# Kernel tuning notes

Measured on AMD Instinct MI355X. Metric: run time of the kernel, lower is better.

## Reference

```python
import jax, jax.numpy as jnp
import numpy as np
from jax import lax

B, T, I, H = 128, 512, 300, 256


def setup_inputs() -> dict:
    key = jax.random.key(0)
    ks = jax.random.split(key, 10)
    k = 1.0 / np.sqrt(H)
    u = lambda kk, shape: jax.random.uniform(kk, shape, jnp.float32, -k, k)
    return {
        "x": jax.random.normal(ks[0], (B, T, I), jnp.float32),
        "W_ih_f": u(ks[1], (4 * H, I)),
        "W_hh_f": u(ks[2], (4 * H, H)),
        "b_f": u(ks[3], (4 * H,)),
        "W_ih_b": u(ks[4], (4 * H, I)),
        "W_hh_b": u(ks[5], (4 * H, H)),
        "b_b": u(ks[6], (4 * H,)),
        "W_lin": u(ks[7], (2, 2 * H)),
        "b_lin": u(ks[8], (2,)),
    }


def _lstm_dir(x, W_ih, W_hh, b, reverse):
    # Precompute input projections for all timesteps: [B, T, 4H]
    xp = jnp.einsum("bti,gi->btg", x, W_ih) + b
    if reverse:
        xp = xp[:, ::-1]
    h0 = jnp.zeros((x.shape[0], H), x.dtype)
    c0 = jnp.zeros((x.shape[0], H), x.dtype)

    def step(carry, xt):
        h, c = carry
        g = xt + h @ W_hh.T  # [B, 4H]
        i_g, f_g, g_g, o_g = jnp.split(g, 4, axis=-1)  # torch gate order i,f,g,o
        i_g = jax.nn.sigmoid(i_g)
        f_g = jax.nn.sigmoid(f_g)
        g_g = jnp.tanh(g_g)
        o_g = jax.nn.sigmoid(o_g)
        c = f_g * c + i_g * g_g
        h = o_g * jnp.tanh(c)
        return (h, c), h

    _, hs = lax.scan(step, (h0, c0), jnp.swapaxes(xp, 0, 1))  # [T, B, H]
    hs = jnp.swapaxes(hs, 0, 1)  # [B, T, H]
    if reverse:
        hs = hs[:, ::-1]
    return hs


def reference(x, W_ih_f, W_hh_f, b_f, W_ih_b, W_hh_b, b_b, W_lin, b_lin):
    hf = _lstm_dir(x, W_ih_f, W_hh_f, b_f, reverse=False)  # [B, T, H]
    hb = _lstm_dir(x, W_ih_b, W_hh_b, b_b, reverse=True)   # [B, T, H]
    last = jnp.concatenate([hf[:, -1], hb[:, -1]], axis=-1)  # [B, 2H]
    return last @ W_lin.T + b_lin  # [B, 2]
```

## Files before the change

kernel.cpp:

```cpp
#include <hip/hip_runtime.h>
#include <cstdint>
#include <cstddef>

typedef _Float16 half2v __attribute__((ext_vector_type(2)));
typedef _Float16 half4v __attribute__((ext_vector_type(4)));
typedef _Float16 half8v __attribute__((ext_vector_type(8)));
typedef float f32x4 __attribute__((ext_vector_type(4)));

#if __has_builtin(__builtin_amdgcn_fdot2)
#define FDOT2(a, b, c) __builtin_amdgcn_fdot2((a), (b), (c), false)
#else
static __device__ __forceinline__ float fdot2_fb(half2v a, half2v b, float c) {
    return c + (float)a[0] * (float)b[0] + (float)a[1] * (float)b[1];
}
#define FDOT2(a, b, c) fdot2_fb((a), (b), (c))
#endif

#define SV2(v, i0, i1) __builtin_shufflevector((v), (v), (i0), (i1))

__device__ __forceinline__ float sigm(float x) { return 1.0f / (1.0f + __expf(-x)); }
__device__ __forceinline__ float tanh_(float x) { return 1.0f - 2.0f / (__expf(2.0f * x) + 1.0f); }

#define BB 128
#define TT 512
#define II 300
#define IIP 320
#define HH 256
#define GG 1024

__global__ __launch_bounds__(256) void cvt_xw(
    const float* __restrict__ X, const float* __restrict__ W,
    _Float16* __restrict__ Xh, _Float16* __restrict__ Wh)
{
    const int total = (65536 + 1024) * 40;
    for (int c = blockIdx.x * 256 + threadIdx.x; c < total; c += gridDim.x * 256) {
        const int row = c / 40;
        const int ch = c - row * 40;
        const int k0 = ch * 8;
        const float* src;
        _Float16* dst;
        if (row < 65536) {
            src = X + (size_t)row * II;
            dst = Xh + (size_t)row * IIP;
        } else {
            src = W + (size_t)(row - 65536) * II;
            dst = Wh + (size_t)(row - 65536) * IIP;
        }
        half8v hv;
        if (k0 + 8 <= II) {
            float4 a = *(const float4*)(src + k0);
            float4 b = *(const float4*)(src + k0 + 4);
            hv = half8v{(_Float16)a.x, (_Float16)a.y, (_Float16)a.z, (_Float16)a.w,
                        (_Float16)b.x, (_Float16)b.y, (_Float16)b.z, (_Float16)b.w};
        } else {
#pragma unroll
            for (int q = 0; q < 8; ++q) {
                const int k = k0 + q;
                hv[q] = (k < II) ? (_Float16)src[k] : (_Float16)0.f;
            }
        }
        *(half8v*)(dst + k0) = hv;
    }
}

#if __has_builtin(__builtin_amdgcn_global_load_lds)
#define HAVE_GLL 1
__device__ __forceinline__ void gll16(const _Float16* g, _Float16* l) {
    __builtin_amdgcn_global_load_lds(
        (const __attribute__((address_space(1))) void*)g,
        (__attribute__((address_space(3))) void*)l, 16, 0, 0);
}
#else
#define HAVE_GLL 0
#endif

__global__ __launch_bounds__(256) void gemm_xp_h(
    const _Float16* __restrict__ Xh, const _Float16* __restrict__ Wh,
    const float* __restrict__ bias, _Float16* __restrict__ XP)
{
    __shared__ __align__(16) _Float16 As[128 * 32];
    __shared__ __align__(16) _Float16 Bs[128 * 32];

    const int t = threadIdx.x;
    const int m0 = blockIdx.y * 128;
    const int n0 = blockIdx.x * 128;
    const int lane = t & 63;
    const int wv = t >> 6;
    const int mq = (wv >> 1) * 4;
    const int nq = (wv & 1) * 4;

    int rowd[2], k4d[2], cidx[2];
#pragma unroll
    for (int r = 0; r < 2; ++r) {
        const int c = wv * 128 + r * 64 + lane;
        cidx[r] = c;
        rowd[r] = ((c >> 6) << 4) | (c & 15);
        k4d[r] = (c >> 4) & 3;
    }

    f32x4 acc[4][4];
#pragma unroll
    for (int i = 0; i < 4; ++i)
#pragma unroll
        for (int j = 0; j < 4; ++j) acc[i][j] = f32x4{0.f, 0.f, 0.f, 0.f};

    for (int kc = 0; kc < IIP; kc += 32) {
        __syncthreads();
#pragma unroll
        for (int r = 0; r < 2; ++r) {
            const _Float16* ga = Xh + (size_t)(m0 + rowd[r]) * IIP + kc + k4d[r] * 8;
            const _Float16* gb = Wh + (size_t)(n0 + rowd[r]) * IIP + kc + k4d[r] * 8;
#if HAVE_GLL
            gll16(ga, &As[cidx[r] * 8]);
            gll16(gb, &Bs[cidx[r] * 8]);
#else
            *(half8v*)(&As[cidx[r] * 8]) = *(const half8v*)ga;
            *(half8v*)(&Bs[cidx[r] * 8]) = *(const half8v*)gb;
#endif
        }
        __syncthreads();

        half8v af[4], bf[4];
#pragma unroll
        for (int i = 0; i < 4; ++i) {
            af[i] = *(const half8v*)(&As[(mq + i) * 512 + (lane >> 4) * 128 + (lane & 15) * 8]);
            bf[i] = *(const half8v*)(&Bs[(nq + i) * 512 + (lane >> 4) * 128 + (lane & 15) * 8]);
        }
#pragma unroll
        for (int i = 0; i < 4; ++i)
#pragma unroll
            for (int j = 0; j < 4; ++j)
                acc[i][j] = __builtin_amdgcn_mfma_f32_16x16x32_f16(af[i], bf[j], acc[i][j], 0, 0, 0);
    }

#pragma unroll
    for (int j = 0; j < 4; ++j) {
        const int n = n0 + (nq + j) * 16 + (lane & 15);
        const float bv = bias[n];
#pragma unroll
        for (int i = 0; i < 4; ++i) {
#pragma unroll
            for (int r = 0; r < 4; ++r) {
                const int m = m0 + (mq + i) * 16 + (lane >> 4) * 4 + r;
                XP[(size_t)m * GG + n] = (_Float16)(acc[i][j][r] + bv);
            }
        }
    }
}

__global__ __launch_bounds__(256, 3) void gemm_xp(
    const float* __restrict__ X, const float* __restrict__ W,
    const float* __restrict__ bias, _Float16* __restrict__ XP)
{
    __shared__ _Float16 As[128 * 32];
    __shared__ _Float16 Bs[128 * 32];

    const int t = threadIdx.x;
    const int m0 = blockIdx.y * 128;
    const int n0 = blockIdx.x * 128;
    const int kpos = t & 7;
    const int rbase = t >> 3;
    const int lane = t & 63;
    const int wv = t >> 6;
    const int mq = (wv >> 1) * 4;
    const int nq = (wv & 1) * 4;

    f32x4 acc[4][4];
#pragma unroll
    for (int i = 0; i < 4; ++i)
#pragma unroll
        for (int j = 0; j < 4; ++j) acc[i][j] = f32x4{0.f, 0.f, 0.f, 0.f};

    for (int kc = 0; kc < 320; kc += 32) {
        __syncthreads();
        const int k0 = kc + kpos * 4;
#pragma unroll
        for (int rr = 0; rr < 4; ++rr) {
            const int row = rbase + rr * 32;
            float4 va = {0.f, 0.f, 0.f, 0.f}, vb = {0.f, 0.f, 0.f, 0.f};
            if (k0 < 300) {
                va = *(const float4*)(X + (size_t)(m0 + row) * II + k0);
                vb = *(const float4*)(W + (size_t)(n0 + row) * II + k0);
            }
            const int idx = (row >> 4) * 512 + (kpos >> 1) * 128 + (row & 15) * 8 + (kpos & 1) * 4;
            half4v ha = {(_Float16)va.x, (_Float16)va.y, (_Float16)va.z, (_Float16)va.w};
            half4v hb = {(_Float16)vb.x, (_Float16)vb.y, (_Float16)vb.z, (_Float16)vb.w};
            *(half4v*)(&As[idx]) = ha;
            *(half4v*)(&Bs[idx]) = hb;
        }
        __syncthreads();

        half8v af[4], bf[4];
#pragma unroll
        for (int i = 0; i < 4; ++i) {
            af[i] = *(const half8v*)(&As[(mq + i) * 512 + (lane >> 4) * 128 + (lane & 15) * 8]);
            bf[i] = *(const half8v*)(&Bs[(nq + i) * 512 + (lane >> 4) * 128 + (lane & 15) * 8]);
        }
#pragma unroll
        for (int i = 0; i < 4; ++i)
#pragma unroll
            for (int j = 0; j < 4; ++j)
                acc[i][j] = __builtin_amdgcn_mfma_f32_16x16x32_f16(af[i], bf[j], acc[i][j], 0, 0, 0);
    }

#pragma unroll
    for (int j = 0; j < 4; ++j) {
        const int n = n0 + (nq + j) * 16 + (lane & 15);
        const float bv = bias[n];
#pragma unroll
        for (int i = 0; i < 4; ++i) {
#pragma unroll
            for (int r = 0; r < 4; ++r) {
                const int m = m0 + (mq + i) * 16 + (lane >> 4) * 4 + r;
                XP[(size_t)m * GG + n] = (_Float16)(acc[i][j][r] + bv);
            }
        }
    }
}

__global__ __attribute__((amdgpu_flat_work_group_size(1024, 1024), amdgpu_waves_per_eu(4, 4)))
void lstm_fwd(
    const float* __restrict__ Whh, const _Float16* __restrict__ XP,
    float* __restrict__ HF)
{
    __shared__ _Float16 wlds[8 * 1024 * 8];
    __shared__ __align__(16) _Float16 hlds[2][HH];

    const int t = threadIdx.x;
    const int b = blockIdx.x;
    const int l = t & 63;
    const int wv = t >> 6;
    const int gate = l >> 4;
    const int j = wv * 16 + (l & 15);
    const int row = gate * 256 + j;
    const bool gb0 = (gate & 1) != 0;
    const bool gb1 = (gate & 2) != 0;

    half2v w[96];
    {
        const float* wr = Whh + (size_t)row * HH;
#pragma unroll
        for (int i = 0; i < 48; ++i) {
            float4 v = *(const float4*)(wr + i * 4);
            w[2 * i]     = half2v{(_Float16)v.x, (_Float16)v.y};
            w[2 * i + 1] = half2v{(_Float16)v.z, (_Float16)v.w};
        }
    }
#pragma unroll
    for (int grp = 0; grp < 8; ++grp) {
        float4 a  = *(const float4*)(Whh + (size_t)t * HH + 192 + grp * 8);
        float4 c4 = *(const float4*)(Whh + (size_t)t * HH + 192 + grp * 8 + 4);
        half8v hv = {(_Float16)a.x, (_Float16)a.y, (_Float16)a.z, (_Float16)a.w,
                     (_Float16)c4.x, (_Float16)c4.y, (_Float16)c4.z, (_Float16)c4.w};
        *(half8v*)(&wlds[grp * 8192 + t * 8]) = hv;
    }
    if (t < HH) hlds[0][t] = (_Float16)0.f;
    float c = 0.0f;
    __syncthreads();

    const _Float16* xq = XP + (size_t)b * TT * GG + row;
    _Float16 x = *xq;

    for (int ts = 0; ts < TT; ++ts) {
        const int p = ts & 1;
        const _Float16* hrd = &hlds[p][0];
        const _Float16* xn = xq + ((ts < TT - 1) ? GG : 0);
        const _Float16 nx = *xn;

        float aLo = 0.f, aHi = 0.f;
#pragma unroll
        for (int cq = 0; cq < 12; ++cq) {
            half8v hv = *(const half8v*)(&hrd[cq * 8]);
            aLo = FDOT2(SV2(hv, 0, 1), w[cq * 4 + 0], aLo);
            aLo = FDOT2(SV2(hv, 2, 3), w[cq * 4 + 1], aLo);
            aLo = FDOT2(SV2(hv, 4, 5), w[cq * 4 + 2], aLo);
            aLo = FDOT2(SV2(hv, 6, 7), w[cq * 4 + 3], aLo);
        }
#pragma unroll
        for (int cq = 12; cq < 24; ++cq) {
            half8v hv = *(const half8v*)(&hrd[cq * 8]);
            aHi = FDOT2(SV2(hv, 0, 1), w[cq * 4 + 0], aHi);
            aHi = FDOT2(SV2(hv, 2, 3), w[cq * 4 + 1], aHi);
            aHi = FDOT2(SV2(hv, 4, 5), w[cq * 4 + 2], aHi);
            aHi = FDOT2(SV2(hv, 6, 7), w[cq * 4 + 3], aHi);
        }
#pragma unroll
        for (int grp = 0; grp < 8; ++grp) {
            half8v hv = *(const half8v*)(&hrd[192 + grp * 8]);
            half8v wl = *(const half8v*)(&wlds[grp * 8192 + row * 8]);
            if (grp & 1) {
                aHi = FDOT2(SV2(hv, 0, 1), SV2(wl, 0, 1), aHi);
                aHi = FDOT2(SV2(hv, 2, 3), SV2(wl, 2, 3), aHi);
                aHi = FDOT2(SV2(hv, 4, 5), SV2(wl, 4, 5), aHi);
                aHi = FDOT2(SV2(hv, 6, 7), SV2(wl, 6, 7), aHi);
            } else {
                aLo = FDOT2(SV2(hv, 0, 1), SV2(wl, 0, 1), aLo);
                aLo = FDOT2(SV2(hv, 2, 3), SV2(wl, 2, 3), aLo);
                aLo = FDOT2(SV2(hv, 4, 5), SV2(wl, 4, 5), aLo);
                aLo = FDOT2(SV2(hv, 6, 7), SV2(wl, 6, 7), aLo);
            }
        }

        const float pre = aLo + aHi + (float)x;
        const float e1 = __shfl_xor(pre, 16, 64);
        const float e2 = __shfl_xor(pre, 32, 64);
        const float e3 = __shfl_xor(pre, 48, 64);
        const float t01 = gb0 ? e1 : pre;
        const float t10 = gb0 ? pre : e1;
        const float t23 = gb0 ? e3 : e2;
        const float t32 = gb0 ? e2 : e3;
        const float gi = gb1 ? t23 : t01;
        const float gf = gb1 ? t32 : t10;
        const float gg = gb1 ? t01 : t23;
        const float go = gb1 ? t10 : t32;

        c = sigm(gf) * c + sigm(gi) * tanh_(gg);
        const float h = sigm(go) * tanh_(c);

        if (gate == 0) {
            hlds[p ^ 1][j] = (_Float16)h;
            if (ts == TT - 1) HF[(size_t)b * HH + j] = h;
        }
        __syncthreads();

        x = nx;
        xq = xn;
    }
}

__global__ __launch_bounds__(256) void lstm_bwd(
    const float* __restrict__ X, const float* __restrict__ Wih,
    const float* __restrict__ bb, float* __restrict__ HB)
{
    __shared__ float xs[II];
    const int b = blockIdx.x, t = threadIdx.x;
    const float* xrow = X + ((size_t)b * TT + (TT - 1)) * II;
    if (t < 75) *(float4*)(&xs[t * 4]) = *(const float4*)(xrow + t * 4);
    __syncthreads();
    if (t < HH) {
        float ai = 0.f, ag = 0.f, ao = 0.f;
        const float4* wi = (const float4*)(Wih + (size_t)t * II);
        const float4* wg = (const float4*)(Wih + (size_t)(t + 512) * II);
        const float4* wo = (const float4*)(Wih + (size_t)(t + 768) * II);
        for (int k4 = 0; k4 < 75; ++k4) {
            float4 xv = *(const float4*)(&xs[k4 * 4]);
            float4 a = wi[k4], g4 = wg[k4], o4 = wo[k4];
            ai += xv.x * a.x + xv.y * a.y + xv.z * a.z + xv.w * a.w;
            ag += xv.x * g4.x + xv.y * g4.y + xv.z * g4.z + xv.w * g4.w;
            ao += xv.x * o4.x + xv.y * o4.y + xv.z * o4.z + xv.w * o4.w;
        }
        ai += bb[t];
        ag += bb[t + 512];
        ao += bb[t + 768];
        const float cg = sigm(ai) * tanh_(ag);
        HB[(size_t)b * HH + t] = sigm(ao) * tanh_(cg);
    }
}

__global__ __launch_bounds__(256) void final_k(
    const float* __restrict__ HF, const float* __restrict__ HB,
    const float* __restrict__ Wlin, const float* __restrict__ blin,
    float* __restrict__ OUT)
{
    const int t = threadIdx.x;
    const int b = t >> 1, jj = t & 1;
    float acc = blin[jj];
    const float* wf = Wlin + jj * 512;
    const float* wb = Wlin + jj * 512 + 256;
    const float* hf = HF + (size_t)b * HH;
    const float* hb = HB + (size_t)b * HH;
    for (int k = 0; k < HH; k += 4) {
        float4 h4 = *(const float4*)(hf + k);
        float4 w4 = *(const float4*)(wf + k);
        float4 g4 = *(const float4*)(hb + k);
        float4 v4 = *(const float4*)(wb + k);
        acc += h4.x * w4.x + h4.y * w4.y + h4.z * w4.z + h4.w * w4.w;
        acc += g4.x * v4.x + g4.y * v4.y + g4.z * v4.z + g4.w * v4.w;
    }
    OUT[b * 2 + jj] = acc;
}

extern "C" void kernel_launch(void* const* d_in, const int* in_sizes, int n_in,
                              void* d_out, int out_size, void* d_ws, size_t ws_size,
                              hipStream_t stream)
{
    const float* x = (const float*)d_in[0];
    const float* Wihf = (const float*)d_in[1];
    const float* Whhf = (const float*)d_in[2];
    const float* bf = (const float*)d_in[3];
    const float* Wihb = (const float*)d_in[4];
    const float* Whhb = (const float*)d_in[5];
    const float* bbv = (const float*)d_in[6];
    const float* Wlin = (const float*)d_in[7];
    const float* blin = (const float*)d_in[8];
    float* out = (float*)d_out;
    (void)Whhb; (void)in_sizes; (void)n_in; (void)out_size;

    const size_t XP_B = (size_t)BB * TT * GG * 2;
    const size_t H_B  = (size_t)BB * HH * 4;
    const size_t XH_B = (size_t)65536 * IIP * 2;
    const size_t WH_B = (size_t)GG * IIP * 2;

    _Float16* xp = (_Float16*)d_ws;
    float* hf = (float*)((char*)d_ws + XP_B);
    float* hb = hf + (size_t)BB * HH;
    _Float16* Xh = (_Float16*)((char*)d_ws + XP_B + 2 * H_B);
    _Float16* Wh = Xh + (size_t)65536 * IIP;

    lstm_bwd<<<BB, 256, 0, stream>>>(x, Wihb, bbv, hb);
    if (ws_size >= XP_B + 2 * H_B + XH_B + WH_B) {
        cvt_xw<<<2048, 256, 0, stream>>>(x, Wihf, Xh, Wh);
        gemm_xp_h<<<dim3(GG / 128, (BB * TT) / 128), 256, 0, stream>>>(Xh, Wh, bf, xp);
    } else {
        gemm_xp<<<dim3(GG / 128, (BB * TT) / 128), 256, 0, stream>>>(x, Wihf, bf, xp);
    }
    lstm_fwd<<<BB, 1024, 0, stream>>>(Whhf, xp, hf);
    final_k<<<1, 256, 0, stream>>>(hf, hb, Wlin, blin, out);
}
```

Before: 1.538 ms.

## Batch 16 sequences per block and compute recurrent matvec with MFMA

The forward LSTM recurrence changes from one batch row per 1024-thread block, using fdot2 dot products, to 16 batch rows per 512-thread block, using 16x16x32 f16 MFMA instructions. Three quarters of W_hh sit in registers as MFMA B fragments and the rest sit in LDS. Hidden state is kept in a swizzled LDS layout, and the gate nonlinearities are applied directly on the accumulator layout. This amortises weight reads over 16 sequences and uses matrix cores, but launches only 8 blocks, so per-step latency on a few CUs now sets the runtime.

```diff
diff --git a/kernel.cpp b/kernel.cpp
--- a/kernel.cpp
+++ b/kernel.cpp
@@ -6,17 +6,6 @@
 typedef _Float16 half4v __attribute__((ext_vector_type(4)));
 typedef _Float16 half8v __attribute__((ext_vector_type(8)));
 typedef float f32x4 __attribute__((ext_vector_type(4)));
-
-#if __has_builtin(__builtin_amdgcn_fdot2)
-#define FDOT2(a, b, c) __builtin_amdgcn_fdot2((a), (b), (c), false)
-#else
-static __device__ __forceinline__ float fdot2_fb(half2v a, half2v b, float c) {
-    return c + (float)a[0] * (float)b[0] + (float)a[1] * (float)b[1];
-}
-#define FDOT2(a, b, c) fdot2_fb((a), (b), (c))
-#endif
-
-#define SV2(v, i0, i1) __builtin_shufflevector((v), (v), (i0), (i1))
 
 __device__ __forceinline__ float sigm(float x) { return 1.0f / (1.0f + __expf(-x)); }
 __device__ __forceinline__ float tanh_(float x) { return 1.0f - 2.0f / (__expf(2.0f * x) + 1.0f); }
@@ -218,113 +207,113 @@
     }
 }
 
-__global__ __attribute__((amdgpu_flat_work_group_size(1024, 1024), amdgpu_waves_per_eu(4, 4)))
+__global__ __attribute__((amdgpu_flat_work_group_size(512, 512), amdgpu_waves_per_eu(2, 2)))
 void lstm_fwd(
     const float* __restrict__ Whh, const _Float16* __restrict__ XP,
     float* __restrict__ HF)
 {
-    __shared__ _Float16 wlds[8 * 1024 * 8];
-    __shared__ __align__(16) _Float16 hlds[2][HH];
+    __shared__ __align__(16) _Float16 wlds[65536];
+    __shared__ __align__(16) _Float16 hl[2][4096];
 
     const int t = threadIdx.x;
-    const int b = blockIdx.x;
+    const int b0 = blockIdx.x * 16;
     const int l = t & 63;
-    const int wv = t >> 6;
-    const int gate = l >> 4;
-    const int j = wv * 16 + (l & 15);
-    const int row = gate * 256 + j;
-    const bool gb0 = (gate & 1) != 0;
-    const bool gb1 = (gate & 2) != 0;
-
-    half2v w[96];
-    {
-        const float* wr = Whh + (size_t)row * HH;
-#pragma unroll
-        for (int i = 0; i < 48; ++i) {
-            float4 v = *(const float4*)(wr + i * 4);
-            w[2 * i]     = half2v{(_Float16)v.x, (_Float16)v.y};
-            w[2 * i + 1] = half2v{(_Float16)v.z, (_Float16)v.w};
-        }
-    }
-#pragma unroll
-    for (int grp = 0; grp < 8; ++grp) {
-        float4 a  = *(const float4*)(Whh + (size_t)t * HH + 192 + grp * 8);
-        float4 c4 = *(const float4*)(Whh + (size_t)t * HH + 192 + grp * 8 + 4);
-        half8v hv = {(_Float16)a.x, (_Float16)a.y, (_Float16)a.z, (_Float16)a.w,
-                     (_Float16)c4.x, (_Float16)c4.y, (_Float16)c4.z, (_Float16)c4.w};
-        *(half8v*)(&wlds[grp * 8192 + t * 8]) = hv;
-    }
-    if (t < HH) hlds[0][t] = (_Float16)0.f;
-    float c = 0.0f;
+    const int w = t >> 6;
+    const int n16 = l & 15;
+    const int kq = l >> 4;
+
+    half8v wr[8][6];
+#pragma unroll
+    for (int ct = 0; ct < 8; ++ct) {
+        const int nct = (ct >> 1) * 256 + w * 32 + (ct & 1) * 16;
+        const float* wp = Whh + (size_t)(nct + n16) * HH + kq * 8;
+#pragma unroll
+        for (int ks = 0; ks < 6; ++ks) {
+            float4 a = *(const float4*)(wp + ks * 32);
+            float4 b = *(const float4*)(wp + ks * 32 + 4);
+            wr[ct][ks] = half8v{(_Float16)a.x, (_Float16)a.y, (_Float16)a.z, (_Float16)a.w,
+                                (_Float16)b.x, (_Float16)b.y, (_Float16)b.z, (_Float16)b.w};
+        }
+    }
+#pragma unroll
+    for (int i = 0; i < 16; ++i) {
+        const int idx = i * 512 + t;
+        const int sn16 = idx & 15;
+        const int skq = (idx >> 4) & 3;
+        const int snt = (idx >> 6) & 63;
+        const int ss  = (idx >> 12) & 1;
+        const float* sp = Whh + (size_t)(snt * 16 + sn16) * HH + (6 + ss) * 32 + skq * 8;
+        float4 a = *(const float4*)sp;
+        float4 b = *(const float4*)(sp + 4);
+        *(half8v*)(&wlds[idx * 8]) = half8v{(_Float16)a.x, (_Float16)a.y, (_Float16)a.z, (_Float16)a.w,
+                                            (_Float16)b.x, (_Float16)b.y, (_Float16)b.z, (_Float16)b.w};
+    }
+#pragma unroll
+    for (int i = 0; i < 8; ++i) hl[0][i * 512 + t] = (_Float16)0.f;
+
+    float cst[8];
+#pragma unroll
+    for (int i = 0; i < 8; ++i) cst[i] = 0.f;
     __syncthreads();
 
-    const _Float16* xq = XP + (size_t)b * TT * GG + row;
-    _Float16 x = *xq;
-
     for (int ts = 0; ts < TT; ++ts) {
-        const int p = ts & 1;
-        const _Float16* hrd = &hlds[p][0];
-        const _Float16* xn = xq + ((ts < TT - 1) ? GG : 0);
-        const _Float16 nx = *xn;
-
-        float aLo = 0.f, aHi = 0.f;
-#pragma unroll
-        for (int cq = 0; cq < 12; ++cq) {
-            half8v hv = *(const half8v*)(&hrd[cq * 8]);
-            aLo = FDOT2(SV2(hv, 0, 1), w[cq * 4 + 0], aLo);
-            aLo = FDOT2(SV2(hv, 2, 3), w[cq * 4 + 1], aLo);
-            aLo = FDOT2(SV2(hv, 4, 5), w[cq * 4 + 2], aLo);
-            aLo = FDOT2(SV2(hv, 6, 7), w[cq * 4 + 3], aLo);
-        }
-#pragma unroll
-        for (int cq = 12; cq < 24; ++cq) {
-            half8v hv = *(const half8v*)(&hrd[cq * 8]);
-            aHi = FDOT2(SV2(hv, 0, 1), w[cq * 4 + 0], aHi);
-            aHi = FDOT2(SV2(hv, 2, 3), w[cq * 4 + 1], aHi);
-            aHi = FDOT2(SV2(hv, 4, 5), w[cq * 4 + 2], aHi);
-            aHi = FDOT2(SV2(hv, 6, 7), w[cq * 4 + 3], aHi);
-        }
-#pragma unroll
-        for (int grp = 0; grp < 8; ++grp) {
-            half8v hv = *(const half8v*)(&hrd[192 + grp * 8]);
-            half8v wl = *(const half8v*)(&wlds[grp * 8192 + row * 8]);
-            if (grp & 1) {
-                aHi = FDOT2(SV2(hv, 0, 1), SV2(wl, 0, 1), aHi);
-                aHi = FDOT2(SV2(hv, 2, 3), SV2(wl, 2, 3), aHi);
-                aHi = FDOT2(SV2(hv, 4, 5), SV2(wl, 4, 5), aHi);
-                aHi = FDOT2(SV2(hv, 6, 7), SV2(wl, 6, 7), aHi);
-            } else {
-                aLo = FDOT2(SV2(hv, 0, 1), SV2(wl, 0, 1), aLo);
-                aLo = FDOT2(SV2(hv, 2, 3), SV2(wl, 2, 3), aLo);
-                aLo = FDOT2(SV2(hv, 4, 5), SV2(wl, 4, 5), aLo);
-                aLo = FDOT2(SV2(hv, 6, 7), SV2(wl, 6, 7), aLo);
-            }
-        }
-
-        const float pre = aLo + aHi + (float)x;
-        const float e1 = __shfl_xor(pre, 16, 64);
-        const float e2 = __shfl_xor(pre, 32, 64);
-        const float e3 = __shfl_xor(pre, 48, 64);
-        const float t01 = gb0 ? e1 : pre;
-        const float t10 = gb0 ? pre : e1;
-        const float t23 = gb0 ? e3 : e2;
-        const float t32 = gb0 ? e2 : e3;
-        const float gi = gb1 ? t23 : t01;
-        const float gf = gb1 ? t32 : t10;
-        const float gg = gb1 ? t01 : t23;
-        const float go = gb1 ? t10 : t32;
-
-        c = sigm(gf) * c + sigm(gi) * tanh_(gg);
-        const float h = sigm(go) * tanh_(c);
-
-        if (gate == 0) {
-            hlds[p ^ 1][j] = (_Float16)h;
-            if (ts == TT - 1) HF[(size_t)b * HH + j] = h;
+        const int cur = ts & 1;
+        const _Float16* hr = &hl[cur][0];
+
+        f32x4 acc[8];
+#pragma unroll
+        for (int ct = 0; ct < 8; ++ct) acc[ct] = f32x4{0.f, 0.f, 0.f, 0.f};
+
+#pragma unroll
+        for (int ks = 0; ks < 6; ++ks) {
+            const int ra = (ks * 512 + kq * 128 + n16 * 8) ^ (kq << 3);
+            half8v A = *(const half8v*)(&hr[ra]);
+#pragma unroll
+            for (int ct = 0; ct < 8; ++ct)
+                acc[ct] = __builtin_amdgcn_mfma_f32_16x16x32_f16(A, wr[ct][ks], acc[ct], 0, 0, 0);
+        }
+#pragma unroll
+        for (int s = 0; s < 2; ++s) {
+            const int ks = 6 + s;
+            const int ra = (ks * 512 + kq * 128 + n16 * 8) ^ (kq << 3);
+            half8v A = *(const half8v*)(&hr[ra]);
+#pragma unroll
+            for (int ct = 0; ct < 8; ++ct) {
+                const int nt = (ct >> 1) * 16 + w * 2 + (ct & 1);
+                half8v Bv = *(const half8v*)(&wlds[(((s * 64 + nt) * 4 + kq) * 16 + n16) * 8]);
+                acc[ct] = __builtin_amdgcn_mfma_f32_16x16x32_f16(A, Bv, acc[ct], 0, 0, 0);
+            }
+        }
+
+        _Float16* hw = &hl[cur ^ 1][0];
+#pragma unroll
+        for (int jt = 0; jt < 2; ++jt) {
+            _Float16 xv[16];
+#pragma unroll
+            for (int r = 0; r < 4; ++r) {
+                const _Float16* xrow = XP + (((size_t)(b0 + kq * 4 + r) * TT) + ts) * GG
+                                          + w * 32 + jt * 16 + n16;
+#pragma unroll
+                for (int g = 0; g < 4; ++g) xv[r * 4 + g] = xrow[g * 256];
+            }
+#pragma unroll
+            for (int r = 0; r < 4; ++r) {
+                const int m = kq * 4 + r;
+                const float gi = acc[0 + jt][r] + (float)xv[r * 4 + 0];
+                const float gf = acc[2 + jt][r] + (float)xv[r * 4 + 1];
+                const float gg = acc[4 + jt][r] + (float)xv[r * 4 + 2];
+                const float go = acc[6 + jt][r] + (float)xv[r * 4 + 3];
+                float cc = cst[jt * 4 + r];
+                cc = sigm(gf) * cc + sigm(gi) * tanh_(gg);
+                cst[jt * 4 + r] = cc;
+                const float h = sigm(go) * tanh_(cc);
+                const int q = (jt * 16 + n16) >> 3;
+                const int logi = w * 512 + q * 128 + m * 8 + (n16 & 7);
+                hw[logi ^ (q << 3)] = (_Float16)h;
+                if (ts == TT - 1) HF[(size_t)(b0 + m) * HH + (w * 32 + jt * 16 + n16)] = h;
+            }
         }
         __syncthreads();
-
-        x = nx;
-        xq = xn;
     }
 }
 
@@ -414,6 +403,6 @@
     } else {
         gemm_xp<<<dim3(GG / 128, (BB * TT) / 128), 256, 0, stream>>>(x, Wihf, bf, xp);
     }
-    lstm_fwd<<<BB, 1024, 0, stream>>>(Whhf, xp, hf);
+    lstm_fwd<<<8, 512, 0, stream>>>(Whhf, xp, hf);
     final_k<<<1, 256, 0, stream>>>(hf, hb, Wlin, blin, out);
 }
```

New measurement: 3.587 ms. 133% more time.
